# Performance work log

Hardware: AMD Instinct MI355X
Metric: run time of the kernel (lower is better)

The kernel has to match this reference:

```python
import jax, jax.numpy as jnp
import numpy as np


def setup_inputs() -> dict:
    key = jax.random.key(0)
    ks = jax.random.split(key, 6)
    B, T, S, H, D, V = 4, 256, 512, 12, 768, 32000
    dec_output = jax.random.normal(ks[0], (B, T, D), dtype=jnp.float32)
    final_output = jax.random.normal(ks[1], (B, T, V), dtype=jnp.float32)
    attention_weights = jax.random.normal(ks[2], (B, H, T, S), dtype=jnp.float32)
    W_pgen = jax.random.normal(ks[3], (D, 1), dtype=jnp.float32) * 0.02
    b_pgen = jnp.zeros((1,), dtype=jnp.float32)
    encoder_input = jax.random.randint(ks[4], (B, S), 0, V, dtype=jnp.int32)
    return {
        "dec_output": dec_output,
        "final_output": final_output,
        "attention_weights": attention_weights,
        "W_pgen": W_pgen,
        "b_pgen": b_pgen,
        "encoder_input": encoder_input,
    }


def reference(dec_output, final_output, attention_weights, W_pgen, b_pgen, encoder_input):
    B, T, V = final_output.shape
    S = encoder_input.shape[1]
    # p_gen = sigmoid(Dense(1)(dec_output)) -> [B, T, 1]
    p_gen = jax.nn.sigmoid(dec_output @ W_pgen + b_pgen)
    # generation distribution
    vocab_dist = p_gen * jax.nn.softmax(final_output, axis=-1)  # [B, T, V]
    # mean over attention heads, then softmax over source positions
    attn = jnp.mean(attention_weights, axis=1)                  # [B, T, S]
    attention_dist = jax.nn.softmax(attn, axis=-1)
    updates = (1.0 - p_gen) * attention_dist                    # [B, T, S]
    # scatter-add attention mass into vocab slots by source token id
    b_idx = jnp.arange(B)[:, None, None]      # [B,1,1]
    t_idx = jnp.arange(T)[None, :, None]      # [1,T,1]
    tok = encoder_input[:, None, :]           # [B,1,S] broadcast over T
    copy_probs = jnp.zeros((B, T, V), dtype=final_output.dtype).at[
        b_idx, t_idx, tok
    ].add(updates)
    combined_probs = vocab_dist + copy_probs
    return jnp.log(combined_probs)
```

## Files before the change

### kernel.cpp

```cpp
#include <hip/hip_runtime.h>
#include <math.h>

namespace {
constexpr int kB = 4, kT = 256, kS = 512, kH = 12, kD = 768, kV = 32000;
constexpr int HASH = 1024;
constexpr int NT = 512;
constexpr int NW = NT / 64;
constexpr int NF4 = kV / 4;
constexpr int FULL = NF4 / NT;
constexpr int REM = NF4 - FULL * NT;

typedef float f32x4 __attribute__((ext_vector_type(4)));

__device__ __forceinline__ f32x4 max4(f32x4 a, f32x4 b) {
  f32x4 o;
  o[0] = fmaxf(a[0], b[0]); o[1] = fmaxf(a[1], b[1]);
  o[2] = fmaxf(a[2], b[2]); o[3] = fmaxf(a[3], b[3]);
  return o;
}
__device__ __forceinline__ void merge2(float& ma, float& sa, float mb, float sb) {
  float mm = fmaxf(ma, mb);
  sa = sa * __expf(ma - mm) + sb * __expf(mb - mm);
  ma = mm;
}
__device__ __forceinline__ float wave_sum(float v) {
  #pragma unroll
  for (int off = 32; off > 0; off >>= 1) v += __shfl_down(v, off, 64);
  return v;
}
__device__ __forceinline__ float wave_max(float v) {
  #pragma unroll
  for (int off = 32; off > 0; off >>= 1) v = fmaxf(v, __shfl_down(v, off, 64));
  return v;
}

__global__ __launch_bounds__(NT, 4) void pg_fused(
    const float* __restrict__ dec_output,
    const float* __restrict__ final_output,
    const float* __restrict__ attn_w,
    const float* __restrict__ W_pgen,
    const float* __restrict__ b_pgen,
    const int*   __restrict__ enc,
    float* __restrict__ out)
{
  const int bt   = blockIdx.x;
  const int b    = bt / kT;
  const int t    = bt - b * kT;
  const int tid  = threadIdx.x;
  const int lane = tid & 63;
  const int wid  = tid >> 6;

  __shared__ int   hkey[HASH];
  __shared__ float hval[HASH];
  __shared__ float redA[NW];
  __shared__ float redm[NW], reds[NW];
  __shared__ float redm2[NW], reds2[NW];

  const float* dec = dec_output + (size_t)bt * kD;
  float d0 = dec[tid] * W_pgen[tid];
  float d1 = (tid < kD - NT) ? dec[tid + NT] * W_pgen[tid + NT] : 0.f;

  float a0 = 0.f;
  #pragma unroll
  for (int hh = 0; hh < kH; ++hh) {
    const float* ap = attn_w + (((size_t)b * kH + hh) * kT + t) * kS;
    a0 += ap[tid];
  }
  const int key = enc[b * kS + tid];
  const float bias = b_pgen[0];

  const f32x4* x4 = (const f32x4*)(final_output + (size_t)bt * kV);
  f32x4 r[FULL + 1];
  #pragma unroll
  for (int k = 0; k < FULL; ++k) r[k] = x4[tid + k * NT];
  const bool has16 = tid < REM;
  if (has16) {
    r[FULL] = x4[tid + FULL * NT];
  } else {
    r[FULL][0] = -INFINITY; r[FULL][1] = -INFINITY;
    r[FULL][2] = -INFINITY; r[FULL][3] = -INFINITY;
  }

  hkey[tid] = -1;        hval[tid] = 0.f;
  hkey[tid + NT] = -1;   hval[tid + NT] = 0.f;

  {
    float acc = wave_sum(d0 + d1);
    if (lane == 0) redA[wid] = acc;
  }
  __syncthreads();

  float z = bias;
  #pragma unroll
  for (int w = 0; w < NW; ++w) z += redA[w];
  const float pg = 1.f / (1.f + expf(-z));

  float val;
  {
    a0 *= (1.f / kH);
    float wm = wave_max(a0);
    if (lane == 0) redm[wid] = wm;
    __syncthreads();
    float mx = redm[0];
    #pragma unroll
    for (int w = 1; w < NW; ++w) mx = fmaxf(mx, redm[w]);
    float e0 = __expf(a0 - mx);
    float ws = wave_sum(e0);
    if (lane == 0) reds[wid] = ws;
    __syncthreads();
    float tot = 0.f;
    #pragma unroll
    for (int w = 0; w < NW; ++w) tot += reds[w];
    val = e0 * ((1.f - pg) / tot);
  }

  {
    unsigned hpos = ((unsigned)key * 2654435761u) >> 22;
    while (true) {
      int prev = atomicCAS(&hkey[hpos], -1, key);
      if (prev == -1 || prev == key) { atomicAdd(&hval[hpos], val); break; }
      hpos = (hpos + 1) & (HASH - 1);
    }
  }

  #pragma unroll
  for (int k = 0; k <= FULL; ++k) {
    asm volatile("" : "+v"(r[k][0]), "+v"(r[k][1]), "+v"(r[k][2]), "+v"(r[k][3]));
  }

  f32x4 mv = r[0];
  #pragma unroll
  for (int k = 1; k <= FULL; ++k) mv = max4(mv, r[k]);
  float m0 = fmaxf(fmaxf(mv[0], mv[1]), fmaxf(mv[2], mv[3]));
  float p0 = 0.f, p1 = 0.f, p2 = 0.f, p3 = 0.f;
  #pragma unroll
  for (int k = 0; k <= FULL; ++k) {
    p0 += __expf(r[k][0] - m0);
    p1 += __expf(r[k][1] - m0);
    p2 += __expf(r[k][2] - m0);
    p3 += __expf(r[k][3] - m0);
  }
  float s0 = (p0 + p1) + (p2 + p3);
  #pragma unroll
  for (int off = 32; off > 0; off >>= 1) {
    float mb = __shfl_down(m0, off, 64);
    float sb = __shfl_down(s0, off, 64);
    merge2(m0, s0, mb, sb);
  }
  if (lane == 0) { redm2[wid] = m0; reds2[wid] = s0; }
  __syncthreads();

  float M = redm2[0], Z = reds2[0];
  #pragma unroll
  for (int w = 1; w < NW; ++w) merge2(M, Z, redm2[w], reds2[w]);
  const float base = logf(pg) - M - logf(Z);

  f32x4* o4 = (f32x4*)(out + (size_t)bt * kV);
  #pragma unroll
  for (int k = 0; k < FULL; ++k)
    __builtin_nontemporal_store(r[k] + base, &o4[tid + k * NT]);
  if (has16)
    __builtin_nontemporal_store(r[FULL] + base, &o4[tid + FULL * NT]);
  __syncthreads();

  {
    const float* xrow = final_output + (size_t)bt * kV;
    float* orow = out + (size_t)bt * kV;
    const float invZ = 1.f / Z;
    for (int i = tid; i < HASH; i += NT) {
      int k2 = hkey[i];
      if (k2 >= 0) {
        float c = hval[i];
        float x = xrow[k2];
        orow[k2] = logf(pg * expf(x - M) * invZ + c);
      }
    }
  }
}
}

extern "C" void kernel_launch(void* const* d_in, const int* in_sizes, int n_in,
                              void* d_out, int out_size, void* d_ws, size_t ws_size,
                              hipStream_t stream) {
  const float* dec = (const float*)d_in[0];
  const float* fin = (const float*)d_in[1];
  const float* aw  = (const float*)d_in[2];
  const float* W   = (const float*)d_in[3];
  const float* bb  = (const float*)d_in[4];
  const int*   enc = (const int*)d_in[5];
  float* out = (float*)d_out;

  pg_fused<<<dim3(kB * kT), dim3(NT), 0, stream>>>(dec, fin, aw, W, bb, enc, out);
}
```

Baseline: 61.75 us.

## Fuse copy-probability fixup into main store using shared vocab bitmap

Adds a shared-memory bitmap marking which vocab ids appear in the encoder input. During the main vectorized output store, each thread checks the bitmap and, for marked slots, looks up the hash table and writes the corrected log-probability directly. This removes the trailing barrier and the second pass of scattered global reads and rewrites of already-stored values. It adds an LDS bitmap read per float4 and divergent hash probes inside the store loop, and it drops the inline-asm register pinning.

New measurement: 109.4 us. 1.77x slower.

```diff
diff --git a/kernel.cpp b/kernel.cpp
--- a/kernel.cpp
+++ b/kernel.cpp
@@ -9,6 +9,7 @@
 constexpr int NF4 = kV / 4;
 constexpr int FULL = NF4 / NT;
 constexpr int REM = NF4 - FULL * NT;
+constexpr int BMPW = kV / 32;
 
 typedef float f32x4 __attribute__((ext_vector_type(4)));
 
@@ -50,11 +51,12 @@
   const int lane = tid & 63;
   const int wid  = tid >> 6;
 
-  __shared__ int   hkey[HASH];
-  __shared__ float hval[HASH];
-  __shared__ float redA[NW];
-  __shared__ float redm[NW], reds[NW];
-  __shared__ float redm2[NW], reds2[NW];
+  __shared__ int      hkey[HASH];
+  __shared__ float    hval[HASH];
+  __shared__ unsigned bmp[BMPW];
+  __shared__ float    redA[NW];
+  __shared__ float    redm[NW], reds[NW];
+  __shared__ float    redm2[NW], reds2[NW];
 
   const float* dec = dec_output + (size_t)bt * kD;
   float d0 = dec[tid] * W_pgen[tid];
@@ -83,6 +85,8 @@
 
   hkey[tid] = -1;        hval[tid] = 0.f;
   hkey[tid + NT] = -1;   hval[tid + NT] = 0.f;
+  bmp[tid] = 0u;
+  if (tid < BMPW - NT) bmp[tid + NT] = 0u;
 
   {
     float acc = wave_sum(d0 + d1);
@@ -121,11 +125,7 @@
       if (prev == -1 || prev == key) { atomicAdd(&hval[hpos], val); break; }
       hpos = (hpos + 1) & (HASH - 1);
     }
-  }
-
-  #pragma unroll
-  for (int k = 0; k <= FULL; ++k) {
-    asm volatile("" : "+v"(r[k][0]), "+v"(r[k][1]), "+v"(r[k][2]), "+v"(r[k][3]));
+    atomicOr(&bmp[(unsigned)key >> 5], 1u << ((unsigned)key & 31));
   }
 
   f32x4 mv = r[0];
@@ -153,28 +153,29 @@
   float M = redm2[0], Z = reds2[0];
   #pragma unroll
   for (int w = 1; w < NW; ++w) merge2(M, Z, redm2[w], reds2[w]);
+  const float invZ = 1.f / Z;
   const float base = logf(pg) - M - logf(Z);
 
   f32x4* o4 = (f32x4*)(out + (size_t)bt * kV);
   #pragma unroll
-  for (int k = 0; k < FULL; ++k)
-    __builtin_nontemporal_store(r[k] + base, &o4[tid + k * NT]);
-  if (has16)
-    __builtin_nontemporal_store(r[FULL] + base, &o4[tid + FULL * NT]);
-  __syncthreads();
-
-  {
-    const float* xrow = final_output + (size_t)bt * kV;
-    float* orow = out + (size_t)bt * kV;
-    const float invZ = 1.f / Z;
-    for (int i = tid; i < HASH; i += NT) {
-      int k2 = hkey[i];
-      if (k2 >= 0) {
-        float c = hval[i];
-        float x = xrow[k2];
-        orow[k2] = logf(pg * expf(x - M) * invZ + c);
+  for (int k = 0; k <= FULL; ++k) {
+    if (k == FULL && !has16) break;
+    const int f = tid + k * NT;
+    f32x4 y = r[k] + base;
+    unsigned w = bmp[f >> 3];
+    unsigned nib = (w >> ((f & 7) * 4)) & 0xFu;
+    if (nib) {
+      #pragma unroll
+      for (int j = 0; j < 4; ++j) {
+        if (nib & (1u << j)) {
+          int vkey = 4 * f + j;
+          unsigned hpos = ((unsigned)vkey * 2654435761u) >> 22;
+          while (hkey[hpos] != vkey) hpos = (hpos + 1) & (HASH - 1);
+          y[j] = logf(pg * __expf(r[k][j] - M) * invZ + hval[hpos]);
+        }
       }
     }
+    __builtin_nontemporal_store(y, &o4[f]);
   }
 }
 }
```
